# Kernel optimization log

Measured on AMD Instinct MI355X. Metric: run time of the kernel, lower is better.

The kernel has to match this reference:

```python
import jax, jax.numpy as jnp
import numpy as np
import math

RCR = 5.2
RCA = 3.5
NUM_SPECIES = 4


def _triu_index(num_species):
    s1, s2 = np.triu_indices(num_species)
    ret = np.zeros((num_species, num_species), dtype=np.int32)
    ret[s1, s2] = np.arange(len(s1))
    ret[s2, s1] = np.arange(len(s1))
    return ret


def _cutoff_cosine(d, rc):
    return 0.5 * jnp.cos(d * (math.pi / rc)) + 0.5


def setup_inputs():
    key = jax.random.key(0)
    k1, k2 = jax.random.split(key)
    M, A = 32, 48
    BOX = 8.0  # ~0.43 atoms/A^3, realistic organic density
    coordinates = jax.random.uniform(k1, (M, A, 3), dtype=jnp.float32) * BOX
    species = jax.random.randint(k2, (M, A), 0, NUM_SPECIES)
    EtaR = jnp.array([16.0], dtype=jnp.float32)
    ShfR = jnp.asarray(0.9 + (RCR - 0.9) / 16.0 * np.arange(16), dtype=jnp.float32)
    EtaA = jnp.array([8.0], dtype=jnp.float32)
    Zeta = jnp.array([32.0], dtype=jnp.float32)
    ShfA = jnp.asarray(0.9 + (RCA - 0.9) / 4.0 * np.arange(4), dtype=jnp.float32)
    ShfZ = jnp.asarray((np.arange(8) + 0.5) * np.pi / 8.0, dtype=jnp.float32)
    return {"coordinates": coordinates, "EtaR": EtaR, "ShfR": ShfR,
            "EtaA": EtaA, "Zeta": Zeta, "ShfA": ShfA, "ShfZ": ShfZ,
            "species": species}


def _compute_aev(coordinates, EtaR, ShfR, EtaA, Zeta, ShfA, ShfZ, species):
    M, A, _ = coordinates.shape
    S = NUM_SPECIES
    npairs_sp = S * (S + 1) // 2  # 10 unordered species pairs
    rad_sub = EtaR.shape[0] * ShfR.shape[0]   # 16
    ang_sub = EtaA.shape[0] * Zeta.shape[0] * ShfA.shape[0] * ShfZ.shape[0]  # 32

    diff = coordinates[:, :, None, :] - coordinates[:, None, :, :]  # (M,A,A,3)
    D = jnp.linalg.norm(diff, axis=-1)                              # (M,A,A)
    mrow = jnp.arange(M)[:, None]

    # ---------- radial AEV (eq. 3) ----------
    p1, p2 = np.triu_indices(A, 1)                                  # static (P,)
    d = D[:, p1, p2]                                                # (M,P)
    mask_r = (d <= RCR).astype(d.dtype)
    du = d[:, :, None, None]                                        # (M,P,1,1)
    fc = _cutoff_cosine(du, RCR)
    rt = 0.25 * jnp.exp(-EtaR[:, None] * (du - ShfR[None, :]) ** 2) * fc
    rt = (rt * mask_r[:, :, None, None]).reshape(M, len(p1), rad_sub)
    sp = species
    idx1 = p1[None, :] * S + sp[:, p2]                              # (M,P)
    idx2 = p2[None, :] * S + sp[:, p1]
    radial = jnp.zeros((M, A * S, rad_sub), dtype=rt.dtype)
    radial = radial.at[mrow, idx1].add(rt).at[mrow, idx2].add(rt)
    radial = radial.reshape(M, A, S * rad_sub)

    # ---------- angular AEV (eq. 4) ----------
    # static triple list: central atom i with unordered neighbor pair (j,k), j,k != i
    jj, kk = np.triu_indices(A - 1, 1)
    tri = []
    for i in range(A):
        others = np.concatenate([np.arange(i), np.arange(i + 1, A)])
        tri.append(np.stack([np.full(jj.shape, i), others[jj], others[kk]], 1))
    tri = np.concatenate(tri)                                       # (T,3)
    ci, n1, n2 = tri[:, 0], tri[:, 1], tri[:, 2]

    v1 = coordinates[:, n1] - coordinates[:, ci]                    # (M,T,3)
    v2 = coordinates[:, n2] - coordinates[:, ci]
    d1 = D[:, ci, n1]
    d2 = D[:, ci, n2]
    mask_a = ((d1 <= RCA) & (d2 <= RCA)).astype(d1.dtype)           # (M,T)
    eps = 1e-8  # torch cosine_similarity eps
    cos = 0.95 * jnp.sum(v1 * v2, -1) / (jnp.maximum(d1, eps) * jnp.maximum(d2, eps))
    ang = jnp.arccos(cos)                                           # (M,T)

    # broadcast axes: (M, T, EtaA, Zeta, ShfA, ShfZ) as in torchani constants
    EtaA_b = EtaA.reshape(1, 1, -1, 1, 1, 1)
    Zeta_b = Zeta.reshape(1, 1, 1, -1, 1, 1)
    ShfA_b = ShfA.reshape(1, 1, 1, 1, -1, 1)
    ShfZ_b = ShfZ.reshape(1, 1, 1, 1, 1, -1)
    a6 = ang[:, :, None, None, None, None]
    dm = ((d1 + d2) / 2)[:, :, None, None, None, None]
    fcj = (_cutoff_cosine(d1, RCA) * _cutoff_cosine(d2, RCA))[:, :, None, None, None, None]
    f1 = ((1 + jnp.cos(a6 - ShfZ_b)) / 2) ** Zeta_b
    f2 = jnp.exp(-EtaA_b * (dm - ShfA_b) ** 2)
    at = (2 * f1 * f2 * fcj).reshape(M, tri.shape[0], ang_sub)
    at = at * mask_a[:, :, None]

    triu = jnp.asarray(_triu_index(S))
    pidx = triu[sp[:, n1], sp[:, n2]]                               # (M,T)
    flat = ci[None, :] * npairs_sp + pidx
    angular = jnp.zeros((M, A * npairs_sp, ang_sub), dtype=at.dtype)
    angular = angular.at[mrow, flat].add(at).reshape(M, A, npairs_sp * ang_sub)

    return jnp.concatenate([radial, angular], axis=-1)              # (M,A,384)


def reference(coordinates, EtaR, ShfR, EtaA, Zeta, ShfA, ShfZ, species):
    return _compute_aev(coordinates, EtaR, ShfR, EtaA, Zeta, ShfA, ShfZ, species)
```

## Files before the change

kernel.cpp:

```cpp
#include <hip/hip_runtime.h>
#include <hip/hip_bf16.h>


#define NA 48
#define RCR_F 5.2f
#define RCA_F 3.5f
#define PI_F 3.14159265358979f
#define RADLEN 64
#define AEVLEN 384

struct Smem {
    float sx[NA], sy[NA], sz[NA];
    int   ssp[NA];
    float rd[NA], rfc[NA];  int rsp[NA];
    float ad[NA], avx[NA], avy[NA], avz[NA], afc[NA]; int asp[NA];
    int   nR, nAn;
    float rpart[4][64];
    float apart[4][320];
};

template <typename T> __device__ __forceinline__ float toF(const T* p, int i);
template <> __device__ __forceinline__ float toF<float>(const float* p, int i) { return p[i]; }
template <> __device__ __forceinline__ float toF<__hip_bfloat16>(const __hip_bfloat16* p, int i) { return __bfloat162float(p[i]); }

template <typename T> __device__ __forceinline__ void stF(T* p, size_t i, float v);
template <> __device__ __forceinline__ void stF<float>(float* p, size_t i, float v) { p[i] = v; }
template <> __device__ __forceinline__ void stF<__hip_bfloat16>(__hip_bfloat16* p, size_t i, float v) { p[i] = __float2bfloat16(v); }

__device__ __forceinline__ int triu_idx(int a, int b) {
    int lo = a < b ? a : b;
    int hi = a < b ? b : a;
    return lo * 4 - (lo * (lo - 1)) / 2 + (hi - lo);
}

template <typename T>
__device__ void aev_body(Smem& sm,
    const T* __restrict__ coords, const T* __restrict__ etaR_p,
    const T* __restrict__ shfR_p, const T* __restrict__ etaA_p,
    const T* __restrict__ zeta_p, const T* __restrict__ shfA_p,
    const T* __restrict__ shfZ_p, const int* __restrict__ species,
    T* __restrict__ out)
{
    const int tid  = threadIdx.x;
    const int lane = tid & 63;
    const int w    = tid >> 6;
    const int bid  = blockIdx.x;
    const int m  = bid / NA;
    const int ci = bid % NA;

    if (tid < NA) {
        int g = m * NA + tid;
        sm.sx[tid]  = toF(coords, 3 * g + 0);
        sm.sy[tid]  = toF(coords, 3 * g + 1);
        sm.sz[tid]  = toF(coords, 3 * g + 2);
        sm.ssp[tid] = species[g];
    }
    __syncthreads();

    if (w == 0) {
        const float cx = sm.sx[ci], cy = sm.sy[ci], cz = sm.sz[ci];
        float dx = 0.f, dy = 0.f, dz = 0.f, d = 1e30f;
        if (lane < NA && lane != ci) {
            dx = sm.sx[lane] - cx; dy = sm.sy[lane] - cy; dz = sm.sz[lane] - cz;
            d = sqrtf(dx * dx + dy * dy + dz * dz);
        }
        unsigned long long mR = __ballot(d <= RCR_F);
        unsigned long long mA = __ballot(d <= RCA_F);
        unsigned long long lanebit = 1ull << lane;
        unsigned long long below = lanebit - 1ull;
        if (mR & lanebit) {
            int s = __popcll(mR & below);
            sm.rd[s]  = d;
            sm.rfc[s] = 0.5f * __cosf(d * (PI_F / RCR_F)) + 0.5f;
            sm.rsp[s] = sm.ssp[lane];
        }
        if (mA & lanebit) {
            int s = __popcll(mA & below);
            sm.ad[s]  = d;
            sm.avx[s] = dx; sm.avy[s] = dy; sm.avz[s] = dz;
            sm.afc[s] = 0.5f * __cosf(d * (PI_F / RCA_F)) + 0.5f;
            sm.asp[s] = sm.ssp[lane];
        }
        if (lane == 0) { sm.nR = (int)__popcll(mR); sm.nAn = (int)__popcll(mA); }
    }
    __syncthreads();

    const int nR  = sm.nR;
    const int nAn = sm.nAn;

    const float etaR = toF(etaR_p, 0);
    const float etaA = toF(etaA_p, 0);
    const float zeta = toF(zeta_p, 0);
    const float myShfR = toF(shfR_p, lane & 15);
    const int   mySp   = lane >> 4;
    const int   myA    = (lane >> 3) & 3;
    const float myShfA = toF(shfA_p, myA);
    const float myShfZ = toF(shfZ_p, lane & 7);
    const float myCz = __cosf(myShfZ);
    const float mySz = __sinf(myShfZ);
    const int   p0   = lane >> 5;
    const bool  z32  = (zeta == 32.f);

    float racc = 0.f;
    for (int i = w; i < nR; i += 4) {
        float df = sm.rd[i] - myShfR;
        float t = 0.25f * __expf(-etaR * df * df) * sm.rfc[i];
        racc += (sm.rsp[i] == mySp) ? t : 0.f;
    }
    sm.rpart[w][lane] = racc;

    float a0 = 0.f, a1 = 0.f, a2 = 0.f, a3 = 0.f, a4 = 0.f;
    const int np = nAn * (nAn - 1) / 2;
    for (int cb = w * 64; cb < np; cb += 256) {
        int p = cb + lane;
        int pp = (p < np) ? p : 0;
        int j = 0, rem = pp, span = nAn - 1;
        while (rem >= span) { rem -= span; span--; j++; }
        int k = j + 1 + rem;
        float d1 = sm.ad[j], d2 = sm.ad[k];
        float dot = sm.avx[j] * sm.avx[k] + sm.avy[j] * sm.avy[k] + sm.avz[j] * sm.avz[k];
        float cv = 0.95f * dot / (fmaxf(d1, 1e-8f) * fmaxf(d2, 1e-8f));
        float sv = sqrtf(fmaxf(1.f - cv * cv, 0.f));
        float dmv = 0.5f * (d1 + d2);
        float fc2 = 2.f * sm.afc[j] * sm.afc[k];
        int   px  = triu_idx(sm.asp[j], sm.asp[k]);

        int cnt = np - cb; if (cnt > 64) cnt = 64;
        for (int q = 0; q < cnt; q++) {
            float qc = __shfl(cv, q);
            float qs = __shfl(sv, q);
            float qd = __shfl(dmv, q);
            float qf = __shfl(fc2, q);
            int   qp = __shfl(px, q);
            float cd = qc * myCz + qs * mySz;
            float x = 0.5f * (1.f + cd);
            float f1;
            if (z32) { float x2 = x*x, x4 = x2*x2, x8 = x4*x4, x16 = x8*x8; f1 = x16*x16; }
            else     { f1 = __powf(x, zeta); }
            float ddm = qd - myShfA;
            float term = f1 * __expf(-etaA * ddm * ddm) * qf;
            a0 += (qp == p0    ) ? term : 0.f;
            a1 += (qp == p0 + 2) ? term : 0.f;
            a2 += (qp == p0 + 4) ? term : 0.f;
            a3 += (qp == p0 + 6) ? term : 0.f;
            a4 += (qp == p0 + 8) ? term : 0.f;
        }
    }
    sm.apart[w][lane + 0]   = a0;
    sm.apart[w][lane + 64]  = a1;
    sm.apart[w][lane + 128] = a2;
    sm.apart[w][lane + 192] = a3;
    sm.apart[w][lane + 256] = a4;
    __syncthreads();

    const size_t ob = (size_t)bid * AEVLEN;
    if (tid < 64) {
        float r = sm.rpart[0][tid] + sm.rpart[1][tid] + sm.rpart[2][tid] + sm.rpart[3][tid];
        stF(out, ob + tid, r);
    }
    {
        float v = sm.apart[0][tid] + sm.apart[1][tid] + sm.apart[2][tid] + sm.apart[3][tid];
        stF(out, ob + RADLEN + tid, v);
    }
    if (tid < 64) {
        int s = 256 + tid;
        float v = sm.apart[0][s] + sm.apart[1][s] + sm.apart[2][s] + sm.apart[3][s];
        stF(out, ob + RADLEN + s, v);
    }
}

__global__ __launch_bounds__(256) void aev_kernel(
    const void* coords, const void* etaR, const void* shfR, const void* etaA,
    const void* zeta, const void* shfA, const void* shfZ,
    const int* __restrict__ species, void* out)
{
    __shared__ Smem sm;
    const float probe = __uint_as_float(((const unsigned int*)shfR)[0]);
    if (probe > 0.85f && probe < 0.95f) {
        aev_body<float>(sm, (const float*)coords, (const float*)etaR,
                        (const float*)shfR, (const float*)etaA, (const float*)zeta,
                        (const float*)shfA, (const float*)shfZ, species, (float*)out);
    } else {
        aev_body<__hip_bfloat16>(sm, (const __hip_bfloat16*)coords,
                        (const __hip_bfloat16*)etaR, (const __hip_bfloat16*)shfR,
                        (const __hip_bfloat16*)etaA, (const __hip_bfloat16*)zeta,
                        (const __hip_bfloat16*)shfA, (const __hip_bfloat16*)shfZ,
                        species, (__hip_bfloat16*)out);
    }
}

extern "C" void kernel_launch(void* const* d_in, const int* in_sizes, int n_in,
                              void* d_out, int out_size, void* d_ws, size_t ws_size,
                              hipStream_t stream) {
    aev_kernel<<<dim3(32 * NA), dim3(256), 0, stream>>>(
        d_in[0], d_in[1], d_in[2], d_in[3], d_in[4], d_in[5], d_in[6],
        (const int*)d_in[7], d_out);
}
```

Measured before the change: 83.52 us.

## Fold angular radial Gaussian and cutoff into exp2 with packed species index

The angular term's exp(-eta*(dm-shfA)^2)*fc2 is expanded algebraically so that the per-pair part, -k*dm^2 + log2(fc2), is computed once per pair. The inner loop then needs a single FMA feeding a native exp2. The species pair index is packed into the low 4 mantissa bits of that per-pair exponent, which cuts the shuffles per inner iteration from five to four. Pair work is also interleaved across waves (p = 4*i + w) instead of contiguous chunks, which should balance the per-wave pair counts. In exchange, the truncated mantissa bits and the log/exp2 path introduce small numerical error, and very small fc2 values are clamped.

```diff
diff --git a/kernel.cpp b/kernel.cpp
--- a/kernel.cpp
+++ b/kernel.cpp
@@ -6,6 +6,7 @@
 #define RCR_F 5.2f
 #define RCA_F 3.5f
 #define PI_F 3.14159265358979f
+#define LOG2E_F 1.44269504088896f
 #define RADLEN 64
 #define AEVLEN 384
 
@@ -100,6 +101,8 @@
     const float mySz = __sinf(myShfZ);
     const int   p0   = lane >> 5;
     const bool  z32  = (zeta == 32.f);
+    const float k2   = etaA * LOG2E_F;
+    const float myLc = k2 * myShfA * myShfA;
 
     float racc = 0.f;
     for (int i = w; i < nR; i += 4) {
@@ -111,34 +114,39 @@
 
     float a0 = 0.f, a1 = 0.f, a2 = 0.f, a3 = 0.f, a4 = 0.f;
     const int np = nAn * (nAn - 1) / 2;
-    for (int cb = w * 64; cb < np; cb += 256) {
-        int p = cb + lane;
-        int pp = (p < np) ? p : 0;
+    const int cnt_w = (np > w) ? ((np - w + 3) >> 2) : 0;
+    for (int base = 0; base < cnt_w; base += 64) {
+        int i = base + lane;
+        int p = 4 * i + w;
+        int pp = (i < cnt_w) ? p : 0;
         int j = 0, rem = pp, span = nAn - 1;
         while (rem >= span) { rem -= span; span--; j++; }
         int k = j + 1 + rem;
         float d1 = sm.ad[j], d2 = sm.ad[k];
         float dot = sm.avx[j] * sm.avx[k] + sm.avy[j] * sm.avy[k] + sm.avz[j] * sm.avz[k];
-        float cv = 0.95f * dot / (fmaxf(d1, 1e-8f) * fmaxf(d2, 1e-8f));
+        float cv = 0.95f * dot / (fmaxf(d1, 1e-8f) * (fmaxf(d2, 1e-8f)));
         float sv = sqrtf(fmaxf(1.f - cv * cv, 0.f));
-        float dmv = 0.5f * (d1 + d2);
+        float dm = 0.5f * (d1 + d2);
         float fc2 = 2.f * sm.afc[j] * sm.afc[k];
-        int   px  = triu_idx(sm.asp[j], sm.asp[k]);
-
-        int cnt = np - cb; if (cnt > 64) cnt = 64;
+        float pe = fmaxf(-k2 * dm * dm + __log2f(fc2), -8.0e4f);
+        float pd = 2.f * k2 * dm;
+        unsigned int pu = (__float_as_uint(pe) & ~15u) | (unsigned)triu_idx(sm.asp[j], sm.asp[k]);
+
+        int cnt = cnt_w - base; if (cnt > 64) cnt = 64;
         for (int q = 0; q < cnt; q++) {
             float qc = __shfl(cv, q);
             float qs = __shfl(sv, q);
-            float qd = __shfl(dmv, q);
-            float qf = __shfl(fc2, q);
-            int   qp = __shfl(px, q);
+            float qd = __shfl(pd, q);
+            unsigned int qu = __shfl((int)pu, q);
+            int   qp  = (int)(qu & 15u);
+            float qpe = __uint_as_float(qu);
             float cd = qc * myCz + qs * mySz;
-            float x = 0.5f * (1.f + cd);
+            float x = 0.5f + 0.5f * cd;
             float f1;
             if (z32) { float x2 = x*x, x4 = x2*x2, x8 = x4*x4, x16 = x8*x8; f1 = x16*x16; }
             else     { f1 = __powf(x, zeta); }
-            float ddm = qd - myShfA;
-            float term = f1 * __expf(-etaA * ddm * ddm) * qf;
+            float f2 = __builtin_amdgcn_exp2f(qd * myShfA + qpe - myLc);
+            float term = f1 * f2;
             a0 += (qp == p0    ) ? term : 0.f;
             a1 += (qp == p0 + 2) ? term : 0.f;
             a2 += (qp == p0 + 4) ? term : 0.f;
```

New measurement: 78.66 us. 1.06x faster.
